# Kernel optimization log

Hardware: AMD Instinct MI355X
Metric: run time of the kernel (lower is better)

Reference implementation:

```python
import jax, jax.numpy as jnp
import numpy as np

B, T, K = 128, 4096, 64
START, STOP = 62, 63
NEG = -10000.0


def setup_inputs() -> dict:
    key = jax.random.key(0)
    k1, k2, k3 = jax.random.split(key, 3)
    feats = jax.random.normal(k1, (B, T, K), dtype=jnp.float32)
    # gold tags never include START/STOP
    tags = jax.random.randint(k2, (B, T), 0, START)
    transitions = jax.random.normal(k3, (K, K), dtype=jnp.float32)
    # mirror the torch __init__ masking: no transition INTO start, none OUT of stop
    transitions = transitions.at[START, :].set(NEG).at[:, STOP].set(NEG)
    return {"feats": feats, "tags": tags, "transitions": transitions}


def _crf_single(feats, tags, transitions):
    """feats: [T,K], tags: [T], transitions: [K,K] (trans[next, prev])."""
    init = jnp.full((K,), NEG, dtype=feats.dtype).at[START].set(0.0)

    # ---- forward algorithm (log partition), vectorized over the tag loop ----
    def fwd_step(alpha, feat):
        # alpha[i] + trans[j, i] + feat[j]  ->  logsumexp over prev i
        new = jax.nn.logsumexp(alpha[None, :] + transitions, axis=1) + feat
        return new, None

    alpha, _ = jax.lax.scan(fwd_step, init, feats)
    forward_score = jax.nn.logsumexp(alpha + transitions[STOP])

    # ---- gold path score (_score_session) ----
    prev_tags = jnp.concatenate([jnp.array([START], dtype=tags.dtype), tags[:-1]])
    emit = jnp.take_along_axis(feats, tags[:, None], axis=1)[:, 0]  # feats[t, tags[t]]
    gold_score = jnp.sum(transitions[tags, prev_tags] + emit) + transitions[STOP, tags[-1]]

    nll = forward_score - gold_score  # neg_log_likelihood

    # ---- Viterbi decode ----
    def vit_step(delta, feat):
        scores = delta[None, :] + transitions  # [next, prev]
        bp = jnp.argmax(scores, axis=1)
        new = jnp.max(scores, axis=1) + feat  # feat added after argmax, as in torch
        return new, bp

    delta, bps = jax.lax.scan(vit_step, init, feats)  # bps: [T, K]
    terminal = delta + transitions[STOP]
    best_last = jnp.argmax(terminal)
    path_score = terminal[best_last]

    def back_step(tag, bp_t):
        return bp_t[tag], tag

    _, best_path = jax.lax.scan(back_step, best_last, bps, reverse=True)  # [T]
    return nll, path_score, best_path


def reference(feats, tags, transitions):
    nll, path_score, best_path = jax.vmap(_crf_single, in_axes=(0, 0, None))(
        feats, tags, transitions
    )
    return nll, path_score, best_path
```

## Files before the change

### kernel.cpp

```cpp
#include <hip/hip_runtime.h>

namespace {
constexpr int Tn = 4096;
constexpr int Kn = 64;
constexpr int BATCH = 128;
constexpr int START_TAG = 62;
constexpr int STOP_TAG = 63;
constexpr float NEGV = -10000.0f;
constexpr int CH = 64;
constexpr int NCH = Tn / CH;
constexpr int GL = 8;
constexpr int NG = Tn / GL;
constexpr int RS = 128;
constexpr int RB = 128;
constexpr int CW = 16;

typedef float f32x4 __attribute__((ext_vector_type(4)));

__device__ __forceinline__ float rfl(float x) {
    return __uint_as_float(__builtin_amdgcn_readfirstlane(__float_as_uint(x)));
}
__device__ __forceinline__ void cfence() { __asm__ volatile("" ::: "memory"); }
__device__ __forceinline__ void lgkm0() { __asm__ volatile("s_waitcnt lgkmcnt(0)" ::: "memory"); }
__device__ __forceinline__ int imin(int a, int b) { return a < b ? a : b; }
__device__ __forceinline__ float m3(float a, float b, float c) {
    return fmaxf(fmaxf(a, b), c);
}

#define DS_WAIT() do {                                                         \
        asm volatile("s_waitcnt lgkmcnt(0)" ::: "memory");                     \
        __builtin_amdgcn_sched_barrier(0);                                     \
    } while (0)

#define DS_PUT(WO, VAL)                                                        \
    asm volatile("ds_write_b32 %0, %1" :: "v"(WO), "v"(VAL) : "memory")

#define DS_GATHER(RO)                                                          \
    asm volatile(                                                              \
        "ds_read_b128 %0, %16 offset:0\n\t"                                    \
        "ds_read_b128 %1, %16 offset:16\n\t"                                   \
        "ds_read_b128 %2, %16 offset:32\n\t"                                   \
        "ds_read_b128 %3, %16 offset:48\n\t"                                   \
        "ds_read_b128 %4, %16 offset:64\n\t"                                   \
        "ds_read_b128 %5, %16 offset:80\n\t"                                   \
        "ds_read_b128 %6, %16 offset:96\n\t"                                   \
        "ds_read_b128 %7, %16 offset:112\n\t"                                  \
        "ds_read_b128 %8, %16 offset:128\n\t"                                  \
        "ds_read_b128 %9, %16 offset:144\n\t"                                  \
        "ds_read_b128 %10, %16 offset:160\n\t"                                 \
        "ds_read_b128 %11, %16 offset:176\n\t"                                 \
        "ds_read_b128 %12, %16 offset:192\n\t"                                 \
        "ds_read_b128 %13, %16 offset:208\n\t"                                 \
        "ds_read_b128 %14, %16 offset:224\n\t"                                 \
        "ds_read_b128 %15, %16 offset:240"                                     \
        : "=&v"(g0), "=&v"(g1), "=&v"(g2), "=&v"(g3),                          \
          "=&v"(g4), "=&v"(g5), "=&v"(g6), "=&v"(g7),                          \
          "=&v"(g8), "=&v"(g9), "=&v"(g10), "=&v"(g11),                        \
          "=&v"(g12), "=&v"(g13), "=&v"(g14), "=&v"(g15)                       \
        : "v"(RO))

__global__ __launch_bounds__(256, 1)
void crf_kernel(const float* __restrict__ feats,
                const int* __restrict__ tags,
                const float* __restrict__ trans,
                float* __restrict__ out,
                unsigned int* __restrict__ bp32)
{
    const int tid = threadIdx.x;
    const int lane = tid & 63;
    const int wid = tid >> 6;
    const int b = blockIdx.x & (BATCH - 1);
    const size_t fb = (size_t)b * Tn * Kn;

    __shared__ float gw[4];
    __shared__ __align__(16) float vbuf[Kn];
    __shared__ __align__(16) float ring_v[RS][Kn];
    __shared__ float ring_m[RS][Kn];
    __shared__ unsigned char ring_bp[RB][Kn];
    __shared__ unsigned char snap[NCH * Kn];
    __shared__ unsigned char echain[NCH];
    __shared__ int prog_a[Kn], prog_b[Kn], prog_c[Kn], prog_d[Kn];
    __shared__ int done_b[Kn], done_c[Kn];

    const unsigned lane4 = (unsigned)lane * 4u;

    if (blockIdx.x < BATCH) {
        float gold = 0.0f;
        {
            const int t0 = tid * (Tn / 256);
            int prev = (tid == 0) ? START_TAG : tags[(size_t)b * Tn + t0 - 1];
            for (int k = 0; k < Tn / 256; ++k) {
                const int t = t0 + k;
                const int tg = tags[(size_t)b * Tn + t];
                gold += trans[tg * Kn + prev] + feats[fb + (size_t)t * Kn + tg];
                prev = tg;
            }
            if (tid == 255) gold += trans[STOP_TAG * Kn + prev];
            #pragma unroll
            for (int off = 32; off; off >>= 1) gold += __shfl_down(gold, off);
            if (lane == 0) gw[wid] = gold;
        }
        __syncthreads();
        if (wid != 0) return;

        float ES[Kn];
        #pragma unroll
        for (int q = 0; q < Kn / 4; ++q) {
            const float4 t4 = ((const float4*)(trans + lane * Kn))[q];
            ES[4*q+0] = __expf(t4.x); ES[4*q+1] = __expf(t4.y);
            ES[4*q+2] = __expf(t4.z); ES[4*q+3] = __expf(t4.w);
        }
        float v = (lane == START_TAG) ? 1.0f : 0.0f;
        float O = 0.0f;
        float fc[GL], fn[GL], Fc[GL];
        #pragma unroll
        for (int k = 0; k < GL; ++k) fc[k] = feats[fb + (size_t)k * Kn + lane];

        const unsigned vb_ro = (unsigned)(size_t)&vbuf[0];
        const unsigned vb_wo = vb_ro + lane4;

        f32x4 g0, g1, g2, g3, g4, g5, g6, g7, g8, g9, g10, g11, g12, g13, g14, g15;
        DS_PUT(vb_wo, v);
        DS_GATHER(vb_ro);

#define FMAQ(Q, A, B2, C, D) ({                                                \
        float s0_ = 0.f, s1_ = 0.f, s2_ = 0.f, s3_ = 0.f;                      \
        s0_ = fmaf(ES[16*(Q)+0],  (A)[0],  s0_); s1_ = fmaf(ES[16*(Q)+1],  (A)[1],  s1_); \
        s2_ = fmaf(ES[16*(Q)+2],  (A)[2],  s2_); s3_ = fmaf(ES[16*(Q)+3],  (A)[3],  s3_); \
        s0_ = fmaf(ES[16*(Q)+4],  (B2)[0], s0_); s1_ = fmaf(ES[16*(Q)+5],  (B2)[1], s1_); \
        s2_ = fmaf(ES[16*(Q)+6],  (B2)[2], s2_); s3_ = fmaf(ES[16*(Q)+7],  (B2)[3], s3_); \
        s0_ = fmaf(ES[16*(Q)+8],  (C)[0],  s0_); s1_ = fmaf(ES[16*(Q)+9],  (C)[1],  s1_); \
        s2_ = fmaf(ES[16*(Q)+10], (C)[2],  s2_); s3_ = fmaf(ES[16*(Q)+11], (C)[3],  s3_); \
        s0_ = fmaf(ES[16*(Q)+12], (D)[0],  s0_); s1_ = fmaf(ES[16*(Q)+13], (D)[1],  s1_); \
        s2_ = fmaf(ES[16*(Q)+14], (D)[2],  s2_); s3_ = fmaf(ES[16*(Q)+15], (D)[3],  s3_); \
        (s0_ + s1_) + (s2_ + s3_); })

#define FWD_STEP(K) do {                                                       \
        DS_WAIT();                                                             \
        const float w0_ = FMAQ(0, g0,  g1,  g2,  g3);                          \
        const float w1_ = FMAQ(1, g4,  g5,  g6,  g7);                          \
        const float w2_ = FMAQ(2, g8,  g9,  g10, g11);                         \
        const float w3_ = FMAQ(3, g12, g13, g14, g15);                         \
        const float w_ = ((w0_ + w1_) + (w2_ + w3_)) * Fc[K];                  \
        const float wz_ = rfl(w_);                                             \
        v = w_ * __builtin_amdgcn_rcpf(wz_);                                   \
        DS_PUT(vb_wo, v);                                                      \
        DS_GATHER(vb_ro);                    \
        O += __logf(wz_);                \
    } while (0)

        for (int g = 0; g < NG; ++g) {
            if (g + 1 < NG) {
                const size_t base = fb + (size_t)(g + 1) * GL * Kn + lane;
                #pragma unroll
                for (int k = 0; k < GL; ++k) fn[k] = feats[base + (size_t)k * Kn];
            }
            #pragma unroll
            for (int k = 0; k < GL; ++k) Fc[k] = __expf(fc[k]);
            #pragma unroll
            for (int k = 0; k < GL; ++k) FWD_STEP(k);
            #pragma unroll
            for (int k = 0; k < GL; ++k) fc[k] = fn[k];
        }
#undef FWD_STEP
        {
            const float a = O + __logf(v);
            const float x = a + trans[STOP_TAG * Kn + lane];
            float mx = x;
            #pragma unroll
            for (int off = 32; off; off >>= 1) mx = fmaxf(mx, __shfl_xor(mx, off));
            float se = __expf(x - mx);
            #pragma unroll
            for (int off = 32; off; off >>= 1) se += __shfl_xor(se, off);
            if (lane == 0)
                out[b] = (mx + __logf(se)) - (((gw[0] + gw[1]) + (gw[2] + gw[3])));
        }
        return;
    }

    volatile int* pa = (volatile int*)prog_a;
    volatile int* pb = (volatile int*)prog_b;
    volatile int* pc = (volatile int*)prog_c;
    volatile int* pd = (volatile int*)prog_d;
    volatile int* db = (volatile int*)done_b;
    volatile int* dc = (volatile int*)done_c;
    if (wid == 0) { pa[lane] = 0; pb[lane] = 0; }
    if (wid == 1) { pc[lane] = 0; pd[lane] = 0; }
    if (wid == 2) { db[lane] = 0; dc[lane] = 0; }
    __syncthreads();

    float trS[Kn];
    #pragma unroll
    for (int q = 0; q < Kn / 4; ++q) {
        const float4 t4 = ((const float4*)(trans + lane * Kn))[q];
        trS[4*q+0] = t4.x; trS[4*q+1] = t4.y; trS[4*q+2] = t4.z; trS[4*q+3] = t4.w;
    }

    if (wid == 0) {
        float v = (lane == START_TAG) ? 0.0f : NEGV;
        float fc[GL], fn[GL];
        #pragma unroll
        for (int k = 0; k < GL; ++k) fc[k] = feats[fb + (size_t)k * Kn + lane];

        const unsigned ring_o = (unsigned)(size_t)&ring_v[0][0];
        f32x4 g0, g1, g2, g3, g4, g5, g6, g7, g8, g9, g10, g11, g12, g13, g14, g15;
        DS_PUT(ring_o + lane4, v);
        DS_GATHER(ring_o);

#define VQ(Q, DV) ({                                                           \
        const float sx_ = (DV)[0] + trS[4*(Q)+0];                              \
        const float sy_ = (DV)[1] + trS[4*(Q)+1];                              \
        const float sz_ = (DV)[2] + trS[4*(Q)+2];                              \
        const float sw_ = (DV)[3] + trS[4*(Q)+3];                              \
        fmaxf(m3(sx_, sy_, sz_), sw_); })

#define VIT_STEP(K) do {                                                       \
        const int t_ = g * GL + (K);                                           \
        DS_WAIT();                                                             \
        const float q0_  = VQ(0,  g0),  q1_  = VQ(1,  g1);                     \
        const float q2_  = VQ(2,  g2),  q3_  = VQ(3,  g3);                     \
        const float q4_  = VQ(4,  g4),  q5_  = VQ(5,  g5);                     \
        const float q6_  = VQ(6,  g6),  q7_  = VQ(7,  g7);                     \
        const float q8_  = VQ(8,  g8),  q9_  = VQ(9,  g9);                     \
        const float q10_ = VQ(10, g10), q11_ = VQ(11, g11);                    \
        const float q12_ = VQ(12, g12), q13_ = VQ(13, g13);                    \
        const float q14_ = VQ(14, g14), q15_ = VQ(15, g15);                    \
        const float r0_ = m3(q0_,  q1_,  q2_);                                 \
        const float r1_ = m3(q3_,  q4_,  q5_);                                 \
        const float r2_ = m3(q6_,  q7_,  q8_);                                 \
        const float r3_ = m3(q9_,  q10_, q11_);                                \
        const float r4_ = m3(q12_, q13_, q14_);                                \
        const float mm_ = fmaxf(m3(m3(r0_, r1_, r2_), r3_, r4_), q15_);        \
        v = mm_ + fc[K];                 \
        const unsigned ro_ = ring_o + (((unsigned)(t_ + 1) & (RS - 1)) << 8);  \
        DS_PUT(ro_ + lane4, v);                                                \
        DS_GATHER(ro_);                      \
        ring_m[t_ & (RS - 1)][lane] = mm_;             \
    } while (0)

        for (int g = 0; g < NG; ++g) {
            if (g + 1 < NG) {
                const size_t base = fb + (size_t)(g + 1) * GL * Kn + lane;
                #pragma unroll
                for (int k = 0; k < GL; ++k) fn[k] = feats[base + (size_t)k * Kn];
            }
            if ((g & 3) == 0 && g >= 16) {
                const int t0 = g * GL;
                cfence();
                while (pb[lane] < t0 - 88 || pc[lane] < t0 - 88)
                    __builtin_amdgcn_s_sleep(1);
                cfence();
            }
            #pragma unroll
            for (int k = 0; k < GL; ++k) VIT_STEP(k);
            cfence();
            pa[lane] = g * GL + GL;
            #pragma unroll
            for (int k = 0; k < GL; ++k) fc[k] = fn[k];
        }
#undef VIT_STEP
#undef VQ
        const float term = v + trans[STOP_TAG * Kn + lane];
        float bv = term;
        int bi = lane;
        #pragma unroll
        for (int off = 32; off; off >>= 1) {
            const float ov = __shfl_xor(bv, off);
            const int oi = __shfl_xor(bi, off);
            if (ov > bv || (ov == bv && oi < bi)) { bv = ov; bi = oi; }
        }
        if (lane == 0) out[BATCH + b] = bv;
        while (pd[lane] < Tn) __builtin_amdgcn_s_sleep(1);
        cfence();
        if (lane == 0) {
            int e = bi;
            for (int c = NCH - 1; c >= 0; --c) {
                echain[c] = (unsigned char)e;
                e = snap[c * Kn + e];
            }
        }
        lgkm0();
        while (db[lane] == 0 || dc[lane] == 0) __builtin_amdgcn_s_sleep(1);
        cfence();
        int tag = echain[lane];
        float* po = out + 2 * BATCH + (size_t)b * Tn;
        const size_t dwb = (size_t)b * (Tn / 4);
        for (int k = CH - 1; k >= 0; --k) {
            const int t = lane * CH + k;
            po[t] = (float)tag;
            tag = (int)((bp32[(dwb + (size_t)(t >> 2)) * Kn + tag] >> (8 * (t & 3))) & 63u);
        }
    } else if (wid == 1 || wid == 2) {
        const int par = wid - 1;
        const size_t dwb = (size_t)b * (Tn / 4);
        volatile int* my = (par == 0) ? pb : pc;
        for (int c0 = par * CW; c0 < Tn; c0 += 2 * CW) {
            while (pa[lane] < c0 + CW) __builtin_amdgcn_s_sleep(1);
            cfence();
            if (c0 >= RB) {
                while (pd[lane] < c0 - (RB - CW)) __builtin_amdgcn_s_sleep(1);
                cfence();
            }
            for (int k4 = 0; k4 < CW; k4 += 4) {
                unsigned int bp4 = 0;
                #pragma unroll
                for (int k = 0; k < 4; ++k) {
                    const int t = c0 + k4 + k;
                    const float4* vp = (const float4*)ring_v[t & (RS - 1)];
                    const float m = ring_m[t & (RS - 1)][lane];
                    int qi[16];
                    #pragma unroll
                    for (int q = 0; q < 16; ++q) {
                        const float4 dv = vp[q];
                        const float sx = dv.x + trS[4*q+0];
                        const float sy = dv.y + trS[4*q+1];
                        const float sz = dv.z + trS[4*q+2];
                        const float sw = dv.w + trS[4*q+3];
                        const int ix = (sx == m) ? 4*q+0 : 255;
                        const int iy = (sy == m) ? 4*q+1 : 255;
                        const int iz = (sz == m) ? 4*q+2 : 255;
                        const int iw = (sw == m) ? 4*q+3 : 255;
                        qi[q] = imin(imin(ix, iy), imin(iz, iw));
                    }
                    int i8[8];
                    #pragma unroll
                    for (int q = 0; q < 8; ++q) i8[q] = imin(qi[2*q], qi[2*q+1]);
                    const int idx = imin(imin(imin(i8[0], i8[1]), imin(i8[2], i8[3])),
                                         imin(imin(i8[4], i8[5]), imin(i8[6], i8[7])));
                    ring_bp[t & (RB - 1)][lane] = (unsigned char)idx;
                    bp4 |= (unsigned int)idx << (8 * k);
                }
                bp32[(dwb + (size_t)((c0 + k4) >> 2)) * Kn + lane] = bp4;
            }
            cfence();
            my[lane] = c0 + CW;
        }
        __asm__ volatile("s_waitcnt vmcnt(0)" ::: "memory");
        if (par == 0) db[lane] = 1; else dc[lane] = 1;
    } else {
        int h = lane;
        for (int c0 = 0; c0 < Tn; c0 += CW) {
            volatile int* pp = ((c0 >> 4) & 1) ? pc : pb;
            while (pp[lane] < c0 + CW) __builtin_amdgcn_s_sleep(1);
            cfence();
            int bpv[CW];
            #pragma unroll
            for (int k = 0; k < CW; ++k)
                bpv[k] = (int)ring_bp[(c0 + k) & (RB - 1)][lane];
            #pragma unroll
            for (int k = 0; k < CW; ++k) h = __shfl(h, bpv[k]);
            if (((c0 >> 4) & 3) == 3) {
                snap[(c0 >> 6) * Kn + lane] = (unsigned char)h;
                h = lane;
            }
            cfence();
            pd[lane] = c0 + CW;
        }
    }
#undef FMAQ
}
}

extern "C" void kernel_launch(void* const* d_in, const int* in_sizes, int n_in,
                              void* d_out, int out_size, void* d_ws, size_t ws_size,
                              hipStream_t stream)
{
    const float* feats = (const float*)d_in[0];
    const int* tags   = (const int*)d_in[1];
    const float* trans = (const float*)d_in[2];
    float* out = (float*)d_out;
    unsigned int* bp = (unsigned int*)d_ws;
    hipLaunchKernelGGL(crf_kernel, dim3(2 * BATCH), dim3(256), 0, stream,
                       feats, tags, trans, out, bp);
}
```

Measured before the change: 1.686 ms.

## Use partial LDS waits in recurrence steps and tree-compose backpointer shuffles

Replaces the single full lgkmcnt(0) wait before each forward and Viterbi step with staged waits (12, 8, 4, 0), so arithmetic on the first gathered quarters can start while later LDS reads are still in flight. The ring_m store now goes through an inline-asm ds_write issued before the ring_v write and gather. The backpointer chain walker composes 16 per-step permutations as a log-depth tree of shuffles instead of a serial chain of dependent shuffles. The staged waits depend on the ds instruction count and ordering matching the counter values, and moving the ring_m write ahead of the gather puts an extra LDS write on the critical path.

```diff
diff --git a/kernel.cpp b/kernel.cpp
--- a/kernel.cpp
+++ b/kernel.cpp
@@ -27,8 +27,8 @@
     return fmaxf(fmaxf(a, b), c);
 }
 
-#define DS_WAIT() do {                                                         \
-        asm volatile("s_waitcnt lgkmcnt(0)" ::: "memory");                     \
+#define DSW(N) do {                                                            \
+        asm volatile("s_waitcnt lgkmcnt(" #N ")" ::: "memory");                \
         __builtin_amdgcn_sched_barrier(0);                                     \
     } while (0)
 
@@ -75,7 +75,7 @@
     __shared__ float gw[4];
     __shared__ __align__(16) float vbuf[Kn];
     __shared__ __align__(16) float ring_v[RS][Kn];
-    __shared__ float ring_m[RS][Kn];
+    __shared__ __align__(16) float ring_m[RS][Kn];
     __shared__ unsigned char ring_bp[RB][Kn];
     __shared__ unsigned char snap[NCH * Kn];
     __shared__ unsigned char echain[NCH];
@@ -136,16 +136,19 @@
         (s0_ + s1_) + (s2_ + s3_); })
 
 #define FWD_STEP(K) do {                                                       \
-        DS_WAIT();                                                             \
+        DSW(12);                                                               \
         const float w0_ = FMAQ(0, g0,  g1,  g2,  g3);                          \
+        DSW(8);                                                                \
         const float w1_ = FMAQ(1, g4,  g5,  g6,  g7);                          \
+        DSW(4);                                                                \
         const float w2_ = FMAQ(2, g8,  g9,  g10, g11);                         \
+        DSW(0);                                                                \
         const float w3_ = FMAQ(3, g12, g13, g14, g15);                         \
         const float w_ = ((w0_ + w1_) + (w2_ + w3_)) * Fc[K];                  \
         const float wz_ = rfl(w_);                                             \
         v = w_ * __builtin_amdgcn_rcpf(wz_);                                   \
         DS_PUT(vb_wo, v);                                                      \
-        DS_GATHER(vb_ro);                    \
+        DS_GATHER(vb_ro);               \
         O += __logf(wz_);                \
     } while (0)
 
@@ -203,6 +206,7 @@
         for (int k = 0; k < GL; ++k) fc[k] = feats[fb + (size_t)k * Kn + lane];
 
         const unsigned ring_o = (unsigned)(size_t)&ring_v[0][0];
+        const unsigned rm_o = (unsigned)(size_t)&ring_m[0][0];
         f32x4 g0, g1, g2, g3, g4, g5, g6, g7, g8, g9, g10, g11, g12, g13, g14, g15;
         DS_PUT(ring_o + lane4, v);
         DS_GATHER(ring_o);
@@ -216,13 +220,16 @@
 
 #define VIT_STEP(K) do {                                                       \
         const int t_ = g * GL + (K);                                           \
-        DS_WAIT();                                                             \
+        DSW(12);                                                               \
         const float q0_  = VQ(0,  g0),  q1_  = VQ(1,  g1);                     \
         const float q2_  = VQ(2,  g2),  q3_  = VQ(3,  g3);                     \
+        DSW(8);                                                                \
         const float q4_  = VQ(4,  g4),  q5_  = VQ(5,  g5);                     \
         const float q6_  = VQ(6,  g6),  q7_  = VQ(7,  g7);                     \
+        DSW(4);                                                                \
         const float q8_  = VQ(8,  g8),  q9_  = VQ(9,  g9);                     \
         const float q10_ = VQ(10, g10), q11_ = VQ(11, g11);                    \
+        DSW(0);                                                                \
         const float q12_ = VQ(12, g12), q13_ = VQ(13, g13);                    \
         const float q14_ = VQ(14, g14), q15_ = VQ(15, g15);                    \
         const float r0_ = m3(q0_,  q1_,  q2_);                                 \
@@ -231,11 +238,12 @@
         const float r3_ = m3(q9_,  q10_, q11_);                                \
         const float r4_ = m3(q12_, q13_, q14_);                                \
         const float mm_ = fmaxf(m3(m3(r0_, r1_, r2_), r3_, r4_), q15_);        \
+        const unsigned mo_ = rm_o + (((unsigned)t_ & (RS - 1)) << 8) + lane4;  \
+        DS_PUT(mo_, mm_);                       \
         v = mm_ + fc[K];                 \
         const unsigned ro_ = ring_o + (((unsigned)(t_ + 1) & (RS - 1)) << 8);  \
         DS_PUT(ro_ + lane4, v);                                                \
-        DS_GATHER(ro_);                      \
-        ring_m[t_ & (RS - 1)][lane] = mm_;             \
+        DS_GATHER(ro_);                  \
     } while (0)
 
         for (int g = 0; g < NG; ++g) {
@@ -347,8 +355,15 @@
             #pragma unroll
             for (int k = 0; k < CW; ++k)
                 bpv[k] = (int)ring_bp[(c0 + k) & (RB - 1)][lane];
-            #pragma unroll
-            for (int k = 0; k < CW; ++k) h = __shfl(h, bpv[k]);
+            const int p0 = __shfl(bpv[0],  bpv[1]),  p1 = __shfl(bpv[2],  bpv[3]);
+            const int p2 = __shfl(bpv[4],  bpv[5]),  p3 = __shfl(bpv[6],  bpv[7]);
+            const int p4 = __shfl(bpv[8],  bpv[9]),  p5 = __shfl(bpv[10], bpv[11]);
+            const int p6 = __shfl(bpv[12], bpv[13]), p7 = __shfl(bpv[14], bpv[15]);
+            const int q0 = __shfl(p0, p1), q1 = __shfl(p2, p3);
+            const int q2 = __shfl(p4, p5), q3 = __shfl(p6, p7);
+            const int r0 = __shfl(q0, q1), r1 = __shfl(q2, q3);
+            const int C = __shfl(r0, r1);
+            h = __shfl(h, C);
             if (((c0 >> 4) & 3) == 3) {
                 snap[(c0 >> 6) * Kn + lane] = (unsigned char)h;
                 h = lane;
```

New measurement: 1.668 ms. No clear change (-1.1%).
